# Performance work log

Measured on AMD Instinct MI355X. Metric: run time of the kernel, lower is better.

## Reference

```python
import jax, jax.numpy as jnp
import numpy as np

INTERP = 10  # gt contour interpolation factor (time=10 in source)
SMOOTH_L1_BETA = 1.0
LOSS_WEIGHT = 1.0


def interpolation(poly):
    # poly: [B, M, 2] -> [B, M*INTERP, 2]
    poly_roll = jnp.roll(poly, shift=1, axis=1)
    step = jnp.arange(INTERP, dtype=poly.dtype) / INTERP  # [INTERP]
    # [B, M, INTERP, 2]
    interp = (poly[:, :, None, :] * step[None, None, :, None]
              + poly_roll[:, :, None, :] * (1.0 - step)[None, None, :, None])
    B, M = poly.shape[0], poly.shape[1]
    return interp.reshape(B, M * INTERP, 2)


def compute_distance(pred, gt):
    # pred: [B, N, 2], gt: [B, M, 2] -> squared euclidean distance [B, M, N]
    # ||g - p||^2 = ||g||^2 + ||p||^2 - 2 g.p  (avoids materializing [B,M,N,2])
    g2 = jnp.sum(gt * gt, axis=-1)[:, :, None]    # [B, M, 1]
    p2 = jnp.sum(pred * pred, axis=-1)[:, None, :]  # [B, 1, N]
    gp = jnp.einsum('bmk,bnk->bmn', gt, pred)
    return g2 + p2 - 2.0 * gp


def smooth_l1(x, y):
    d = jnp.abs(x - y)
    return jnp.where(d < SMOOTH_L1_BETA, 0.5 * d * d / SMOOTH_L1_BETA, d - 0.5 * SMOOTH_L1_BETA)


def setup_inputs() -> dict:
    key = jax.random.key(0)
    k1, k2, k3, k4 = jax.random.split(key, 4)
    B, N, M = 1024, 128, 128
    ini_pred_poly = jax.random.normal(k1, (B, N, 2), dtype=jnp.float32)
    pred_poly = ini_pred_poly + 0.1 * jax.random.normal(k2, (B, N, 2), dtype=jnp.float32)
    gt_poly = jax.random.normal(k3, (B, M, 2), dtype=jnp.float32)
    keyPointsMask = (jax.random.uniform(k4, (B, M)) < 0.7).astype(jnp.float32)
    return {'ini_pred_poly': ini_pred_poly, 'pred_poly': pred_poly,
            'gt_poly': gt_poly, 'keyPointsMask': keyPointsMask}


def reference(ini_pred_poly, pred_poly, gt_poly, keyPointsMask):
    # --- lossPred2NearestGt ---
    gt_interp = interpolation(gt_poly)                       # [B, M*10, 2]
    d1 = compute_distance(ini_pred_poly, gt_interp)          # [B, M*10, N]
    index_gt = jnp.argmin(d1, axis=1)                        # [B, N]
    nearest_gt = jnp.take_along_axis(gt_interp, index_gt[:, :, None], axis=1)  # [B, N, 2]
    loss_pred2gt = jnp.mean(smooth_l1(pred_poly, nearest_gt))  # scalar (reduction='mean')

    # --- lossGt2NearestPred ---
    d2 = compute_distance(ini_pred_poly, gt_poly)            # [B, M, N]
    index_pred = jnp.argmin(d2, axis=2)                      # [B, M]
    nearest_pred = jnp.take_along_axis(pred_poly, index_pred[:, :, None], axis=1)  # [B, M, 2]
    loss_gt2pred = smooth_l1(nearest_pred, gt_poly)          # [B, M, 2] (reduction='none')

    # mask expanded to [B, M, 2] in the source -> its sum counts both coords
    mask = keyPointsMask[:, :, None]
    masked_sum = jnp.sum(loss_gt2pred * mask)
    mask_sum = 2.0 * jnp.sum(keyPointsMask)
    loss_set2set = masked_sum / (mask_sum + 1.0) + loss_pred2gt
    loss = loss_set2set / 2.0
    return LOSS_WEIGHT * loss
```

## Files before the change

### kernel.cpp

```cpp
#include <hip/hip_runtime.h>
#include <math.h>


#define BB    1024
#define NN    128
#define MM    128

__device__ __forceinline__ float sl1(float x) {
    float d = fabsf(x);
    return d < 1.0f ? 0.5f * d * d : d - 0.5f;
}

__global__ void __launch_bounds__(512, 8)
dmloss_main(const float* __restrict__ ini, const float* __restrict__ pred,
            const float* __restrict__ gt,  const float* __restrict__ kmask,
            float4* __restrict__ partials)
{
    const int b   = blockIdx.x;
    const int tid = threadIdx.x;
    const int n   = tid & 127;
    const int h   = tid >> 7;

    __shared__ float2 s_gt[MM];
    __shared__ float4 s_ii[NN];
    __shared__ float2 s_pr[NN];
    __shared__ float4 s_segA[MM];
    __shared__ float4 s_segB[MM];
    __shared__ float  s_step[16];
    __shared__ float  s_rv[512];
    __shared__ float  s_rf[512];
    __shared__ float  s_sum[3][8];

    const float2* gt2 = (const float2*)(gt   + (size_t)b * MM * 2);
    const float2* in2 = (const float2*)(ini  + (size_t)b * NN * 2);
    const float2* pr2 = (const float2*)(pred + (size_t)b * NN * 2);

    float2 myPr = make_float2(0.f, 0.f);
    float  myKm = 0.f;

    if (tid < 128) {
        s_gt[tid] = gt2[tid];
        myPr = pr2[tid];
        myKm = kmask[b * MM + tid];
    } else if (tid < 256) {
        int k = tid - 128;
        float2 p = in2[k];
        s_ii[k] = make_float4(p.x, p.y, (float)k, 0.0f);
    } else if (tid < 384) {
        int k = tid - 256;
        s_pr[k] = pr2[k];
    } else if (tid < 400) {
        int j = tid - 384;
        s_step[j] = (float)j / 10.0f;
    }
    __syncthreads();

    if (tid < 128) {
        float2 a  = s_gt[(tid + 127) & 127];
        float2 gm = s_gt[tid];
        float ex = gm.x - a.x, ey = gm.y - a.y;
        float A  = ex * ex + ey * ey;
        float inv = 10.0f / A;
        float exi = ex * inv, eyi = ey * inv;
        float aei = -(a.x * exi + a.y * eyi);
        s_segA[tid] = make_float4(a.x, a.y, ex, ey);
        s_segB[tid] = make_float4(exi, eyi, aei, (float)(tid * 10));
    }
    __syncthreads();

    float4 I0 = s_ii[n];
    const float px = I0.x, py = I0.y;
    float sumA = 0.0f, sumB = 0.0f, sumC = 0.0f;

    float best = INFINITY, bf = 1e30f;
    {
        #pragma unroll 4
        for (int m = h; m < MM; m += 4) {
            float4 T2 = s_segB[m];
            float4 T1 = s_segA[m];
            float jv = fmaf(px, T2.x, fmaf(py, T2.y, T2.z));
            float jc = fminf(fmaxf(jv, 0.0f), 9.0f);
            float jr = rintf(jc);
            float s  = jr * 0.1f;
            float gx = fmaf(T1.z, s, T1.x);
            float gy = fmaf(T1.w, s, T1.y);
            float dx = gx - px, dy = gy - py;
            float d  = fmaf(dx, dx, dy * dy);
            float fi = T2.w + jr;
            bool better = d < best;
            best = better ? d : best;
            bf   = better ? fi : bf;
        }
        s_rv[tid] = best; s_rf[tid] = bf;
    }
    __syncthreads();
    if (h == 0) {
        #pragma unroll
        for (int q = 1; q < 4; ++q) {
            float ov = s_rv[n + 128 * q];
            float of = s_rf[n + 128 * q];
            if (ov < best || (ov == best && of < bf)) { best = ov; bf = of; }
        }
        int bidx = (int)bf;
        int m = bidx / 10;
        int j = bidx - m * 10;
        float s = s_step[j];
        float t = 1.0f - s;
        float2 gm = s_gt[m];
        float2 gp = s_gt[(m + 127) & 127];
        float gx = gm.x * s + gp.x * t;
        float gy = gm.y * s + gp.y * t;
        sumA = sl1(myPr.x - gx) + sl1(myPr.y - gy);
    }
    __syncthreads();

    {
        float2 g = s_gt[n];
        best = INFINITY; bf = 1e30f;
        #pragma unroll 4
        for (int k = h; k < NN; k += 4) {
            float4 Ik = s_ii[k];
            float dx = Ik.x - g.x, dy = Ik.y - g.y;
            float d  = fmaf(dx, dx, dy * dy);
            bool better = d < best;
            best = better ? d : best;
            bf   = better ? Ik.z : bf;
        }
        s_rv[tid] = best; s_rf[tid] = bf;
        __syncthreads();
        if (h == 0) {
            #pragma unroll
            for (int q = 1; q < 4; ++q) {
                float ov = s_rv[n + 128 * q];
                float of = s_rf[n + 128 * q];
                if (ov < best || (ov == best && of < bf)) { best = ov; bf = of; }
            }
            int k = (int)bf;
            float2 pk = s_pr[k];
            sumB = myKm * (sl1(pk.x - g.x) + sl1(pk.y - g.y));
            sumC = myKm;
        }
    }

    #pragma unroll
    for (int off = 32; off > 0; off >>= 1) {
        sumA += __shfl_down(sumA, off);
        sumB += __shfl_down(sumB, off);
        sumC += __shfl_down(sumC, off);
    }
    const int wave = tid >> 6, lane = tid & 63;
    if (lane == 0) {
        s_sum[0][wave] = sumA; s_sum[1][wave] = sumB; s_sum[2][wave] = sumC;
    }
    __syncthreads();
    if (tid == 0) {
        float A = 0.0f, Bs = 0.0f, C = 0.0f;
        #pragma unroll
        for (int w = 0; w < 8; ++w) {
            A += s_sum[0][w]; Bs += s_sum[1][w]; C += s_sum[2][w];
        }
        partials[b] = make_float4(A, Bs, C, 0.0f);
    }
}

__global__ void __launch_bounds__(256)
dmloss_final(const float4* __restrict__ partials, float* __restrict__ out)
{
    const int tid = threadIdx.x;
    float A = 0.0f, Bs = 0.0f, C = 0.0f;
    #pragma unroll
    for (int i = tid; i < BB; i += 256) {
        float4 p = partials[i];
        A += p.x; Bs += p.y; C += p.z;
    }
    #pragma unroll
    for (int off = 32; off > 0; off >>= 1) {
        A  += __shfl_down(A, off);
        Bs += __shfl_down(Bs, off);
        C  += __shfl_down(C, off);
    }
    __shared__ float sA[4], sB[4], sC[4];
    const int wave = tid >> 6, lane = tid & 63;
    if (lane == 0) { sA[wave] = A; sB[wave] = Bs; sC[wave] = C; }
    __syncthreads();
    if (tid == 0) {
        float a  = sA[0] + sA[1] + sA[2] + sA[3];
        float bs = sB[0] + sB[1] + sB[2] + sB[3];
        float c  = sC[0] + sC[1] + sC[2] + sC[3];
        float loss_pred2gt = a / ((float)BB * (float)NN * 2.0f);
        float loss_set2set = bs / (2.0f * c + 1.0f) + loss_pred2gt;
        out[0] = 0.5f * loss_set2set;
    }
}

extern "C" void kernel_launch(void* const* d_in, const int* in_sizes, int n_in,
                              void* d_out, int out_size, void* d_ws, size_t ws_size,
                              hipStream_t stream)
{
    const float* ini   = (const float*)d_in[0];
    const float* pred  = (const float*)d_in[1];
    const float* gt    = (const float*)d_in[2];
    const float* kmask = (const float*)d_in[3];
    float4* partials = (float4*)d_ws;

    dmloss_main<<<dim3(BB), dim3(512), 0, stream>>>(ini, pred, gt, kmask, partials);
    dmloss_final<<<dim3(1), dim3(256), 0, stream>>>(partials, (float*)d_out);
}
```

Measured before the change: 19.62 us.

## Fuse final reduction via last-block atomic counter and use packed-FP32 readlane inner loops

Replaces the separate final-reduction kernel with a last-block-done pattern: each block stores its partials atomically, bumps a global counter, and the last block reduces everything and writes the loss. The two nearest-point searches are rewritten so segment and point data are held in registers and broadcast with readlane, with two candidates handled at once through v_pk_* FP32 instructions. The point-to-segment distance uses an expanded algebraic form instead of rebuilding the point, which removes the LDS tables and one sync. The trade-off is an added memset launch and atomics, plus possible small numeric differences from the expanded distance formula.

```diff
diff --git a/kernel.cpp b/kernel.cpp
--- a/kernel.cpp
+++ b/kernel.cpp
@@ -2,10 +2,24 @@
 #include <math.h>
 
 
-#define BB    1024
-#define NN    128
-#define MM    128
-
+#define BB 1024
+#define NN 128
+#define MM 128
+
+typedef float v2f __attribute__((ext_vector_type(2)));
+
+__device__ __forceinline__ v2f pk_add(v2f a, v2f b) {
+    v2f d; asm("v_pk_add_f32 %0, %1, %2" : "=v"(d) : "v"(a), "v"(b)); return d;
+}
+__device__ __forceinline__ v2f pk_mul(v2f a, v2f b) {
+    v2f d; asm("v_pk_mul_f32 %0, %1, %2" : "=v"(d) : "v"(a), "v"(b)); return d;
+}
+__device__ __forceinline__ v2f pk_fma(v2f a, v2f b, v2f c) {
+    v2f d; asm("v_pk_fma_f32 %0, %1, %2, %3" : "=v"(d) : "v"(a), "v"(b), "v"(c)); return d;
+}
+__device__ __forceinline__ float rdl(float v, int l) {
+    return __builtin_bit_cast(float, __builtin_amdgcn_readlane(__builtin_bit_cast(int, v), l));
+}
 __device__ __forceinline__ float sl1(float x) {
     float d = fabsf(x);
     return d < 1.0f ? 0.5f * d * d : d - 0.5f;
@@ -14,22 +28,23 @@
 __global__ void __launch_bounds__(512, 8)
 dmloss_main(const float* __restrict__ ini, const float* __restrict__ pred,
             const float* __restrict__ gt,  const float* __restrict__ kmask,
-            float4* __restrict__ partials)
+            float* __restrict__ pA, float* __restrict__ pB, float* __restrict__ pC,
+            unsigned* __restrict__ counter, float* __restrict__ out)
 {
-    const int b   = blockIdx.x;
-    const int tid = threadIdx.x;
-    const int n   = tid & 127;
-    const int h   = tid >> 7;
+    const int b    = blockIdx.x;
+    const int tid  = threadIdx.x;
+    const int n    = tid & 127;
+    const int h    = tid >> 7;
+    const int lane = tid & 63;
+    const int u    = lane & 15;
 
     __shared__ float2 s_gt[MM];
-    __shared__ float4 s_ii[NN];
     __shared__ float2 s_pr[NN];
-    __shared__ float4 s_segA[MM];
-    __shared__ float4 s_segB[MM];
     __shared__ float  s_step[16];
     __shared__ float  s_rv[512];
     __shared__ float  s_rf[512];
     __shared__ float  s_sum[3][8];
+    __shared__ int    s_last;
 
     const float2* gt2 = (const float2*)(gt   + (size_t)b * MM * 2);
     const float2* in2 = (const float2*)(ini  + (size_t)b * NN * 2);
@@ -37,64 +52,82 @@
 
     float2 myPr = make_float2(0.f, 0.f);
     float  myKm = 0.f;
-
     if (tid < 128) {
         s_gt[tid] = gt2[tid];
         myPr = pr2[tid];
         myKm = kmask[b * MM + tid];
     } else if (tid < 256) {
-        int k = tid - 128;
-        float2 p = in2[k];
-        s_ii[k] = make_float4(p.x, p.y, (float)k, 0.0f);
-    } else if (tid < 384) {
-        int k = tid - 256;
-        s_pr[k] = pr2[k];
-    } else if (tid < 400) {
-        int j = tid - 384;
-        s_step[j] = (float)j / 10.0f;
-    }
-    __syncthreads();
-
-    if (tid < 128) {
-        float2 a  = s_gt[(tid + 127) & 127];
-        float2 gm = s_gt[tid];
-        float ex = gm.x - a.x, ey = gm.y - a.y;
-        float A  = ex * ex + ey * ey;
-        float inv = 10.0f / A;
-        float exi = ex * inv, eyi = ey * inv;
-        float aei = -(a.x * exi + a.y * eyi);
-        s_segA[tid] = make_float4(a.x, a.y, ex, ey);
-        s_segB[tid] = make_float4(exi, eyi, aei, (float)(tid * 10));
-    }
-    __syncthreads();
-
-    float4 I0 = s_ii[n];
-    const float px = I0.x, py = I0.y;
-    float sumA = 0.0f, sumB = 0.0f, sumC = 0.0f;
-
-    float best = INFINITY, bf = 1e30f;
+        s_pr[tid - 128] = pr2[tid - 128];
+    } else if (tid < 272) {
+        s_step[tid - 256] = (float)(tid - 256) / 10.0f;
+    }
+
+    const int kA = h + 8 * u;
+    float2 p  = in2[n];
+    float2 iA = in2[kA];
+    float2 iB = in2[kA + 4];
+    const float px = p.x, py = p.y;
+    v2f cix = { iA.x, iB.x };
+    v2f ciy = { iA.y, iB.y };
+    __syncthreads();
+
+    v2f cax, cay, cex, cey, cE;
     {
-        #pragma unroll 4
-        for (int m = h; m < MM; m += 4) {
-            float4 T2 = s_segB[m];
-            float4 T1 = s_segA[m];
-            float jv = fmaf(px, T2.x, fmaf(py, T2.y, T2.z));
-            float jc = fminf(fmaxf(jv, 0.0f), 9.0f);
-            float jr = rintf(jc);
-            float s  = jr * 0.1f;
-            float gx = fmaf(T1.z, s, T1.x);
-            float gy = fmaf(T1.w, s, T1.y);
-            float dx = gx - px, dy = gy - py;
-            float d  = fmaf(dx, dx, dy * dy);
-            float fi = T2.w + jr;
-            bool better = d < best;
-            best = better ? d : best;
-            bf   = better ? fi : bf;
-        }
+        float2 aA = s_gt[(kA + 127) & 127];
+        float2 gA = s_gt[kA];
+        float2 aB = s_gt[kA + 3];
+        float2 gB = s_gt[kA + 4];
+        float exA = gA.x - aA.x, eyA = gA.y - aA.y;
+        float exB = gB.x - aB.x, eyB = gB.y - aB.y;
+        float AA = exA * exA + eyA * eyA;
+        float AB = exB * exB + eyB * eyB;
+        float invA = AA > 0.f ? 10.f / AA : 0.f;
+        float invB = AB > 0.f ? 10.f / AB : 0.f;
+        cax = (v2f){ aA.x, aB.x };
+        cay = (v2f){ aA.y, aB.y };
+        cex = (v2f){ -exA * invA, -exB * invB };
+        cey = (v2f){ -eyA * invA, -eyB * invB };
+        cE  = (v2f){ AA * 0.01f, AB * 0.01f };
+    }
+
+    const v2f pxn = { -px, -px };
+    const v2f pyn = { -py, -py };
+    const v2f m2  = { -2.f, -2.f };
+    float sumA = 0.f, sumB = 0.f, sumC = 0.f;
+
+    float dE = INFINITY, dO = INFINITY;
+    float cdE = 0.f, cdO = 0.f, jrE = 0.f, jrO = 0.f;
+    #pragma unroll
+    for (int t = 0; t < 16; ++t) {
+        v2f ax, ay, ex, ey, E;
+        ax.x = rdl(cax.x, t); ax.y = rdl(cax.y, t);
+        ay.x = rdl(cay.x, t); ay.y = rdl(cay.y, t);
+        ex.x = rdl(cex.x, t); ex.y = rdl(cex.y, t);
+        ey.x = rdl(cey.x, t); ey.y = rdl(cey.y, t);
+        E.x  = rdl(cE.x,  t); E.y  = rdl(cE.y,  t);
+        v2f qx = pk_add(ax, pxn);
+        v2f qy = pk_add(ay, pyn);
+        v2f jv = pk_fma(qy, ey, pk_mul(qx, ex));
+        v2f jr;
+        jr.x = rintf(fminf(fmaxf(jv.x, 0.f), 9.f));
+        jr.y = rintf(fminf(fmaxf(jv.y, 0.f), 9.f));
+        v2f q2 = pk_fma(qy, qy, pk_mul(qx, qx));
+        v2f t2 = pk_fma(jv, m2, jr);
+        v2f d2 = pk_fma(pk_mul(E, jr), t2, q2);
+        if (d2.x < dE) { dE = d2.x; cdE = (float)t; jrE = jr.x; }
+        if (d2.y < dO) { dO = d2.y; cdO = (float)t; jrO = jr.y; }
+    }
+    {
+        float hb  = (float)(10 * h);
+        float fiE = fmaf(80.f, cdE, hb + jrE);
+        float fiO = fmaf(80.f, cdO, hb + 40.f + jrO);
+        float best = dE, bf = fiE;
+        if (dO < best || (dO == best && fiO < bf)) { best = dO; bf = fiO; }
         s_rv[tid] = best; s_rf[tid] = bf;
     }
     __syncthreads();
     if (h == 0) {
+        float best = s_rv[tid], bf = s_rf[tid];
         #pragma unroll
         for (int q = 1; q < 4; ++q) {
             float ov = s_rv[n + 128 * q];
@@ -105,39 +138,51 @@
         int m = bidx / 10;
         int j = bidx - m * 10;
         float s = s_step[j];
-        float t = 1.0f - s;
+        float tt = 1.0f - s;
         float2 gm = s_gt[m];
         float2 gp = s_gt[(m + 127) & 127];
-        float gx = gm.x * s + gp.x * t;
-        float gy = gm.y * s + gp.y * t;
+        float gx = gm.x * s + gp.x * tt;
+        float gy = gm.y * s + gp.y * tt;
         sumA = sl1(myPr.x - gx) + sl1(myPr.y - gy);
     }
     __syncthreads();
 
     {
         float2 g = s_gt[n];
-        best = INFINITY; bf = 1e30f;
-        #pragma unroll 4
-        for (int k = h; k < NN; k += 4) {
-            float4 Ik = s_ii[k];
-            float dx = Ik.x - g.x, dy = Ik.y - g.y;
-            float d  = fmaf(dx, dx, dy * dy);
-            bool better = d < best;
-            best = better ? d : best;
-            bf   = better ? Ik.z : bf;
-        }
+        const v2f gxn = { -g.x, -g.x };
+        const v2f gyn = { -g.y, -g.y };
+        float d2E = INFINITY, d2O = INFINITY;
+        float c2E = 0.f, c2O = 0.f;
+        #pragma unroll
+        for (int t = 0; t < 16; ++t) {
+            v2f ix, iy;
+            ix.x = rdl(cix.x, t); ix.y = rdl(cix.y, t);
+            iy.x = rdl(ciy.x, t); iy.y = rdl(ciy.y, t);
+            v2f dx = pk_add(ix, gxn);
+            v2f dy = pk_add(iy, gyn);
+            v2f d2 = pk_fma(dy, dy, pk_mul(dx, dx));
+            if (d2.x < d2E) { d2E = d2.x; c2E = (float)t; }
+            if (d2.y < d2O) { d2O = d2.y; c2O = (float)t; }
+        }
+        float hf = (float)h;
+        float fE = fmaf(8.f, c2E, hf);
+        float fO = fmaf(8.f, c2O, hf + 4.f);
+        float best = d2E, bf = fE;
+        if (d2O < best || (d2O == best && fO < bf)) { best = d2O; bf = fO; }
         s_rv[tid] = best; s_rf[tid] = bf;
         __syncthreads();
         if (h == 0) {
+            float2 g0 = s_gt[tid];
+            float bst = s_rv[tid], bfi = s_rf[tid];
             #pragma unroll
             for (int q = 1; q < 4; ++q) {
                 float ov = s_rv[n + 128 * q];
                 float of = s_rf[n + 128 * q];
-                if (ov < best || (ov == best && of < bf)) { best = ov; bf = of; }
+                if (ov < bst || (ov == bst && of < bfi)) { bst = ov; bfi = of; }
             }
-            int k = (int)bf;
-            float2 pk = s_pr[k];
-            sumB = myKm * (sl1(pk.x - g.x) + sl1(pk.y - g.y));
+            int k = (int)bfi;
+            float2 pk2 = s_pr[k];
+            sumB = myKm * (sl1(pk2.x - g0.x) + sl1(pk2.y - g0.y));
             sumC = myKm;
         }
     }
@@ -148,48 +193,54 @@
         sumB += __shfl_down(sumB, off);
         sumC += __shfl_down(sumC, off);
     }
-    const int wave = tid >> 6, lane = tid & 63;
-    if (lane == 0) {
+    const int wave = tid >> 6;
+    if ((tid & 63) == 0) {
         s_sum[0][wave] = sumA; s_sum[1][wave] = sumB; s_sum[2][wave] = sumC;
     }
     __syncthreads();
     if (tid == 0) {
-        float A = 0.0f, Bs = 0.0f, C = 0.0f;
+        float A = 0.f, Bs = 0.f, C = 0.f;
         #pragma unroll
         for (int w = 0; w < 8; ++w) {
             A += s_sum[0][w]; Bs += s_sum[1][w]; C += s_sum[2][w];
         }
-        partials[b] = make_float4(A, Bs, C, 0.0f);
-    }
-}
-
-__global__ void __launch_bounds__(256)
-dmloss_final(const float4* __restrict__ partials, float* __restrict__ out)
-{
-    const int tid = threadIdx.x;
-    float A = 0.0f, Bs = 0.0f, C = 0.0f;
-    #pragma unroll
-    for (int i = tid; i < BB; i += 256) {
-        float4 p = partials[i];
-        A += p.x; Bs += p.y; C += p.z;
-    }
-    #pragma unroll
-    for (int off = 32; off > 0; off >>= 1) {
-        A  += __shfl_down(A, off);
-        Bs += __shfl_down(Bs, off);
-        C  += __shfl_down(C, off);
-    }
-    __shared__ float sA[4], sB[4], sC[4];
-    const int wave = tid >> 6, lane = tid & 63;
-    if (lane == 0) { sA[wave] = A; sB[wave] = Bs; sC[wave] = C; }
-    __syncthreads();
-    if (tid == 0) {
-        float a  = sA[0] + sA[1] + sA[2] + sA[3];
-        float bs = sB[0] + sB[1] + sB[2] + sB[3];
-        float c  = sC[0] + sC[1] + sC[2] + sC[3];
-        float loss_pred2gt = a / ((float)BB * (float)NN * 2.0f);
-        float loss_set2set = bs / (2.0f * c + 1.0f) + loss_pred2gt;
-        out[0] = 0.5f * loss_set2set;
+        __hip_atomic_store(&pA[b], A,  __ATOMIC_RELAXED, __HIP_MEMORY_SCOPE_AGENT);
+        __hip_atomic_store(&pB[b], Bs, __ATOMIC_RELAXED, __HIP_MEMORY_SCOPE_AGENT);
+        __hip_atomic_store(&pC[b], C,  __ATOMIC_RELAXED, __HIP_MEMORY_SCOPE_AGENT);
+        unsigned prev = __hip_atomic_fetch_add(counter, 1u, __ATOMIC_ACQ_REL,
+                                               __HIP_MEMORY_SCOPE_AGENT);
+        s_last = (prev == (unsigned)(BB - 1));
+    }
+    __syncthreads();
+
+    if (s_last) {
+        float A = 0.f, Bs = 0.f, C = 0.f;
+        #pragma unroll
+        for (int i = tid; i < BB; i += 512) {
+            A  += __hip_atomic_load(&pA[i], __ATOMIC_RELAXED, __HIP_MEMORY_SCOPE_AGENT);
+            Bs += __hip_atomic_load(&pB[i], __ATOMIC_RELAXED, __HIP_MEMORY_SCOPE_AGENT);
+            C  += __hip_atomic_load(&pC[i], __ATOMIC_RELAXED, __HIP_MEMORY_SCOPE_AGENT);
+        }
+        #pragma unroll
+        for (int off = 32; off > 0; off >>= 1) {
+            A  += __shfl_down(A, off);
+            Bs += __shfl_down(Bs, off);
+            C  += __shfl_down(C, off);
+        }
+        if ((tid & 63) == 0) {
+            s_sum[0][wave] = A; s_sum[1][wave] = Bs; s_sum[2][wave] = C;
+        }
+        __syncthreads();
+        if (tid == 0) {
+            float a = 0.f, bs = 0.f, c = 0.f;
+            #pragma unroll
+            for (int w = 0; w < 8; ++w) {
+                a += s_sum[0][w]; bs += s_sum[1][w]; c += s_sum[2][w];
+            }
+            float loss_pred2gt = a / ((float)BB * (float)NN * 2.0f);
+            float loss_set2set = bs / (2.0f * c + 1.0f) + loss_pred2gt;
+            out[0] = 0.5f * loss_set2set;
+        }
     }
 }
 
@@ -201,8 +252,14 @@
     const float* pred  = (const float*)d_in[1];
     const float* gt    = (const float*)d_in[2];
     const float* kmask = (const float*)d_in[3];
-    float4* partials = (float4*)d_ws;
-
-    dmloss_main<<<dim3(BB), dim3(512), 0, stream>>>(ini, pred, gt, kmask, partials);
-    dmloss_final<<<dim3(1), dim3(256), 0, stream>>>(partials, (float*)d_out);
-}
+
+    float*    pA      = (float*)d_ws;
+    float*    pB      = pA + BB;
+    float*    pC      = pB + BB;
+    unsigned* counter = (unsigned*)(pC + BB);
+
+    hipMemsetAsync(counter, 0, sizeof(unsigned), stream);
+    dmloss_main<<<dim3(BB), dim3(512), 0, stream>>>(ini, pred, gt, kmask,
+                                                    pA, pB, pC, counter,
+                                                    (float*)d_out);
+}
```

Measured after the change: 38.68 us. +97.1%, slower.
